# Optimization experiments

Hardware: AMD Instinct MI355X
Metric: run time of the kernel (lower is better)

Reference implementation:

```python
import jax, jax.numpy as jnp
import numpy as np

P_DROP = 0.3
TEMP = 1.0
UNC_THRESH = 0.3
TOP_K = 2
EXTRA_K = 2  # min(2, num_experts - top_k)
NUM_SAMPLES = 5


def setup_inputs() -> dict:
    key = jax.random.key(0)
    ks = jax.random.split(key, 7)
    B, D, H, E = 16384, 4096, 128, 64
    return {
        "x": jax.random.normal(ks[0], (B, D), jnp.float32),
        "W1": jax.random.normal(ks[1], (D, H), jnp.float32) / np.sqrt(D),
        "b1": jnp.zeros((H,), jnp.float32),
        "W2": jax.random.normal(ks[2], (H, E), jnp.float32) / np.sqrt(H),
        "b2": jnp.zeros((E,), jnp.float32),
        "mask1_u": jax.random.uniform(ks[3], (NUM_SAMPLES, B, H), jnp.float32),
        "mask2_u": jax.random.uniform(ks[4], (NUM_SAMPLES, B, E), jnp.float32),
    }


def reference(x, W1, b1, W2, b2, mask1_u, mask2_u):
    scale = 1.0 / (1.0 - P_DROP)
    # layer1: Linear -> ReLU -> Dropout; W1 is shared, so compute once and
    # apply per-sample dropout masks (identical math to the torch loop).
    h = jax.nn.relu(x @ W1 + b1)                              # [B, H]
    h = h[None] * ((mask1_u >= P_DROP).astype(h.dtype) * scale)  # [S, B, H]
    # layer2: Linear -> Dropout
    logits = jnp.einsum("sbh,he->sbe", h, W2) + b2            # [S, B, E]
    logits = logits * ((mask2_u >= P_DROP).astype(logits.dtype) * scale)

    mean_logits = logits.mean(axis=0)                          # [B, E]
    probs = jax.nn.softmax(mean_logits / TEMP, axis=-1)        # [B, E]
    all_probs = jax.nn.softmax(logits / TEMP, axis=-1)         # [S, B, E]
    # torch .std() is unbiased (ddof=1)
    uncertainty = jnp.std(all_probs, axis=0, ddof=1).mean(axis=-1)  # [B]

    # top_k + conditional expansion by EXTRA_K when uncertain.
    full_probs, full_idx = jax.lax.top_k(probs, TOP_K + EXTRA_K)
    topk_probs, topk_idx = full_probs[:, :TOP_K], full_idx[:, :TOP_K]
    uncertain = (uncertainty > UNC_THRESH)[:, None]
    extra_probs = jnp.where(uncertain, full_probs[:, TOP_K:], 0.0)
    extra_idx = jnp.where(uncertain, full_idx[:, TOP_K:], -1)
    out_idx = jnp.concatenate([topk_idx, extra_idx], axis=1)       # [B, TOP_K+EXTRA_K]
    out_probs = jnp.concatenate([topk_probs, extra_probs], axis=1)
    return out_idx, out_probs, uncertainty
```

## Files before the change

kernel.cpp:

```cpp
#include <hip/hip_runtime.h>

typedef short short8 __attribute__((ext_vector_type(8)));
typedef float f32x4 __attribute__((ext_vector_type(4)));

#define B_ROWS 16384
#define SCALE 1.4285714285714286f

__device__ __forceinline__ float bf2f(unsigned short u) {
    return __uint_as_float(((unsigned)u) << 16);
}
__device__ __forceinline__ unsigned short f2bf(float f) {
    unsigned u = __float_as_uint(f);
    u += 0x7fffu + ((u >> 16) & 1u);
    return (unsigned short)(u >> 16);
}

__device__ __forceinline__ void gl_lds16(const void* g, void* l) {
    __builtin_amdgcn_global_load_lds(
        (const __attribute__((address_space(1))) unsigned int*)g,
        (__attribute__((address_space(3))) unsigned int*)l, 16, 0, 0);
}

__device__ __forceinline__ float wave_max(float v) {
    #pragma unroll
    for (int m = 1; m < 64; m <<= 1) v = fmaxf(v, __shfl_xor(v, m, 64));
    return v;
}
__device__ __forceinline__ float wave_sum(float v) {
    #pragma unroll
    for (int m = 1; m < 64; m <<= 1) v += __shfl_xor(v, m, 64);
    return v;
}

__global__ void k_prep(const float* __restrict__ w1,
                       unsigned short* __restrict__ w1h,
                       unsigned short* __restrict__ w1l) {
    int tid = blockIdx.x * 256 + threadIdx.x;
    int n = tid >> 12, k = tid & 4095;
    float v = w1[k * 128 + n];
    unsigned short hi = f2bf(v);
    w1h[tid] = hi;
    w1l[tid] = f2bf(v - bf2f(hi));
}

__global__ __launch_bounds__(256) void k_gemm(const float* __restrict__ x,
                                              const unsigned short* __restrict__ w1h,
                                              const unsigned short* __restrict__ w1l,
                                              const float* __restrict__ b1,
                                              float* __restrict__ hout) {
    __shared__ unsigned short sAh[2][32 * 64], sAl[2][32 * 64];
    __shared__ unsigned short sBh[2][128 * 64], sBl[2][128 * 64];
    const int t = threadIdx.x;
    const int w = t >> 6, lane = t & 63;
    const int l15 = lane & 15, l4 = lane >> 4;
    const int rowBase = blockIdx.x << 5;

    f32x4 acc[2][2];
    #pragma unroll
    for (int i = 0; i < 2; ++i)
        #pragma unroll
        for (int j = 0; j < 2; ++j) {
            f32x4 z = {0.f, 0.f, 0.f, 0.f};
            acc[i][j] = z;
        }

    const int am = t >> 3, as = t & 7;
    const int apc = as ^ (am & 7);

    auto stage = [&](int buf, int k0) {
        #pragma unroll
        for (int j = 0; j < 4; ++j) {
            int c = j * 256 + t;
            int n = c >> 3;
            int cl = (c & 7) ^ (n & 7);
            const size_t go = (size_t)n * 4096 + k0 + (cl << 3);
            gl_lds16(w1h + go, &sBh[buf][c << 3]);
            gl_lds16(w1l + go, &sBl[buf][c << 3]);
        }
        const float* src = x + ((size_t)(rowBase + am) << 12) + k0 + (as << 3);
        float4 a0 = *(const float4*)src;
        float4 a1 = *(const float4*)(src + 4);
        float av[8] = {a0.x, a0.y, a0.z, a0.w, a1.x, a1.y, a1.z, a1.w};
        short8 H, L;
        #pragma unroll
        for (int i = 0; i < 8; ++i) {
            unsigned short hi = f2bf(av[i]);
            H[i] = (short)hi;
            L[i] = (short)f2bf(av[i] - bf2f(hi));
        }
        *(short8*)&sAh[buf][((am << 3) + apc) << 3] = H;
        *(short8*)&sAl[buf][((am << 3) + apc) << 3] = L;
    };

    stage(0, 0);
    __syncthreads();
    for (int it = 0; it < 64; ++it) {
        int buf = it & 1;
        if (it + 1 < 64) stage(buf ^ 1, (it + 1) << 6);
        #pragma unroll
        for (int ks = 0; ks < 2; ++ks) {
            short8 ah[2], al[2], bh[2], bl[2];
            #pragma unroll
            for (int mf = 0; mf < 2; ++mf) {
                int rm = (mf << 4) + l15;
                int pc = ((ks << 2) + l4) ^ (rm & 7);
                ah[mf] = *(const short8*)&sAh[buf][(((rm << 3) + pc)) << 3];
                al[mf] = *(const short8*)&sAl[buf][(((rm << 3) + pc)) << 3];
            }
            #pragma unroll
            for (int nf = 0; nf < 2; ++nf) {
                int rn = (w << 5) + (nf << 4) + l15;
                int pc = ((ks << 2) + l4) ^ (rn & 7);
                bh[nf] = *(const short8*)&sBh[buf][(((rn << 3) + pc)) << 3];
                bl[nf] = *(const short8*)&sBl[buf][(((rn << 3) + pc)) << 3];
            }
            #pragma unroll
            for (int mf = 0; mf < 2; ++mf)
                #pragma unroll
                for (int nf = 0; nf < 2; ++nf) {
                    acc[mf][nf] = __builtin_amdgcn_mfma_f32_16x16x32_bf16(
                        ah[mf], bh[nf], acc[mf][nf], 0, 0, 0);
                    acc[mf][nf] = __builtin_amdgcn_mfma_f32_16x16x32_bf16(
                        ah[mf], bl[nf], acc[mf][nf], 0, 0, 0);
                    acc[mf][nf] = __builtin_amdgcn_mfma_f32_16x16x32_bf16(
                        al[mf], bh[nf], acc[mf][nf], 0, 0, 0);
                }
        }
        __syncthreads();
    }

    #pragma unroll
    for (int nf = 0; nf < 2; ++nf) {
        int col = (w << 5) + (nf << 4) + l15;
        float bias = b1[col];
        #pragma unroll
        for (int mf = 0; mf < 2; ++mf) {
            int r0 = rowBase + (mf << 4) + (l4 << 2);
            #pragma unroll
            for (int rr = 0; rr < 4; ++rr) {
                float v = acc[mf][nf][rr] + bias;
                hout[(size_t)(r0 + rr) * 128 + col] = v > 0.f ? v : 0.f;
            }
        }
    }
}

__global__ __launch_bounds__(640) void k_logits(const float* __restrict__ h,
                                                const float* __restrict__ w2,
                                                const float* __restrict__ b2,
                                                const float* __restrict__ m1,
                                                const float* __restrict__ m2,
                                                float* __restrict__ lg) {
    const int t = threadIdx.x;
    const int wave = t >> 6, lane = t & 63;
    const int eh = (wave >= 5) ? 1 : 0;
    const int s = wave - (eh ? 5 : 0);
    const int row = (blockIdx.x << 6) + lane;
    const int ebu = __builtin_amdgcn_readfirstlane(eh << 5);

    float acc[32];
    #pragma unroll
    for (int e = 0; e < 32; ++e) acc[e] = 0.f;

    const float* hp = h + (size_t)row * 128;
    const float* m1p = m1 + ((size_t)s * B_ROWS + row) * 128;
    const float* wp = w2 + ebu;

    for (int k = 0; k < 128; k += 4) {
        float4 h4 = *(const float4*)(hp + k);
        float4 mu = *(const float4*)(m1p + k);
        float hd0 = (mu.x >= 0.3f) ? h4.x * SCALE : 0.f;
        float hd1 = (mu.y >= 0.3f) ? h4.y * SCALE : 0.f;
        float hd2 = (mu.z >= 0.3f) ? h4.z * SCALE : 0.f;
        float hd3 = (mu.w >= 0.3f) ? h4.w * SCALE : 0.f;
        const float* wk = wp + (k << 6);
        #pragma unroll
        for (int e = 0; e < 32; ++e) acc[e] += hd0 * wk[e];
        #pragma unroll
        for (int e = 0; e < 32; ++e) acc[e] += hd1 * wk[64 + e];
        #pragma unroll
        for (int e = 0; e < 32; ++e) acc[e] += hd2 * wk[128 + e];
        #pragma unroll
        for (int e = 0; e < 32; ++e) acc[e] += hd3 * wk[192 + e];
    }

    const float* m2p = m2 + ((size_t)s * B_ROWS + row) * 64 + ebu;
    float* op = lg + ((size_t)s * B_ROWS + row) * 64 + ebu;
    #pragma unroll
    for (int e = 0; e < 32; ++e) {
        float lv = acc[e] + b2[ebu + e];
        acc[e] = (m2p[e] >= 0.3f) ? lv * SCALE : 0.f;
    }
    #pragma unroll
    for (int e = 0; e < 32; e += 4) {
        float4 v = make_float4(acc[e], acc[e + 1], acc[e + 2], acc[e + 3]);
        *(float4*)(op + e) = v;
    }
}

__global__ __launch_bounds__(256) void k_stats(const float* __restrict__ lg,
                                               float* __restrict__ out) {
    const int lane = threadIdx.x & 63;
    const int wv = threadIdx.x >> 6;
    const int row = (blockIdx.x << 2) + wv;

    float l[5], p[5];
    #pragma unroll
    for (int s = 0; s < 5; ++s)
        l[s] = lg[((size_t)s * B_ROWS + row) * 64 + lane];

    float ml = (((l[0] + l[1]) + l[2]) + l[3] + l[4]);
    ml = ((((l[0] + l[1]) + l[2]) + l[3]) + l[4]) / 5.0f;

    #pragma unroll
    for (int s = 0; s < 5; ++s) {
        float mx = wave_max(l[s]);
        float ev = expf(l[s] - mx);
        float sm = wave_sum(ev);
        p[s] = ev / sm;
    }

    float mx = wave_max(ml);
    float ev = expf(ml - mx);
    float sm = wave_sum(ev);
    float prob = ev / sm;

    float mean = ((((p[0] + p[1]) + p[2]) + p[3]) + p[4]) / 5.0f;
    float var = 0.f;
    #pragma unroll
    for (int s = 0; s < 5; ++s) { float d = p[s] - mean; var += d * d; }
    float sd = sqrtf(var * 0.25f);
    float unc = wave_sum(sd) / 64.0f;

    float pv = prob;
    float vv[4]; int vi[4];
    #pragma unroll
    for (int t4 = 0; t4 < 4; ++t4) {
        float bv = pv; int bi = lane;
        #pragma unroll
        for (int m = 1; m < 64; m <<= 1) {
            float ov = __shfl_xor(bv, m, 64);
            int oi = __shfl_xor(bi, m, 64);
            if (ov > bv || (ov == bv && oi < bi)) { bv = ov; bi = oi; }
        }
        vv[t4] = bv; vi[t4] = bi;
        if (lane == bi) pv = -1.f;
    }

    if (lane == 0) {
        bool ug = unc > 0.3f;
        float4 fi = make_float4((float)vi[0], (float)vi[1],
                                ug ? (float)vi[2] : -1.f,
                                ug ? (float)vi[3] : -1.f);
        *(float4*)(out + (size_t)row * 4) = fi;
        float4 fp = make_float4(vv[0], vv[1],
                                ug ? vv[2] : 0.f,
                                ug ? vv[3] : 0.f);
        *(float4*)(out + 65536 + (size_t)row * 4) = fp;
        out[131072 + row] = unc;
    }
}

extern "C" void kernel_launch(void* const* d_in, const int* in_sizes, int n_in,
                              void* d_out, int out_size, void* d_ws, size_t ws_size,
                              hipStream_t stream) {
    const float* x  = (const float*)d_in[0];
    const float* W1 = (const float*)d_in[1];
    const float* b1 = (const float*)d_in[2];
    const float* W2 = (const float*)d_in[3];
    const float* b2 = (const float*)d_in[4];
    const float* m1 = (const float*)d_in[5];
    const float* m2 = (const float*)d_in[6];
    float* out = (float*)d_out;
    char* ws = (char*)d_ws;

    unsigned short* w1h = (unsigned short*)ws;
    unsigned short* w1l = (unsigned short*)(ws + (1 << 20));
    float* h  = (float*)(ws + (2 << 20));
    float* lg = (float*)(ws + (10 << 20));

    k_prep  <<<2048, 256, 0, stream>>>(W1, w1h, w1l);
    k_gemm  <<<512,  256, 0, stream>>>(x, w1h, w1l, b1, h);
    k_logits<<<256,  640, 0, stream>>>(h, W2, b2, m1, m2, lg);
    k_stats <<<4096, 256, 0, stream>>>(lg, out);
}
```

Measured before the change: 497.6 us.

## Fuse logits and stats kernels, stage per-sample logits in LDS

Merges the layer-2 logits kernel and the softmax/uncertainty/top-k kernel into one kernel that keeps each block's 32 rows × 5 samples of logits in shared memory. This removes the global write and re-read of the [5,B,64] logits buffer and one kernel launch. The thread mapping also changes: each thread now handles one row and 8 experts across all 5 samples, so each h value is reused across samples. In exchange, grid size drops to 512 blocks of 256 threads, the block uses 40KB of LDS, and the stats phase runs rows sequentially per wave, which may reduce parallelism.

```diff
diff --git a/kernel.cpp b/kernel.cpp
--- a/kernel.cpp
+++ b/kernel.cpp
@@ -145,119 +145,135 @@
     }
 }
 
-__global__ __launch_bounds__(640) void k_logits(const float* __restrict__ h,
-                                                const float* __restrict__ w2,
-                                                const float* __restrict__ b2,
-                                                const float* __restrict__ m1,
-                                                const float* __restrict__ m2,
-                                                float* __restrict__ lg) {
+__global__ __launch_bounds__(256) void k_logstats(const float* __restrict__ h,
+                                                  const float* __restrict__ w2,
+                                                  const float* __restrict__ b2,
+                                                  const float* __restrict__ m1,
+                                                  const float* __restrict__ m2,
+                                                  float* __restrict__ out) {
+    __shared__ float lgs[5 * 32 * 64];
     const int t = threadIdx.x;
-    const int wave = t >> 6, lane = t & 63;
-    const int eh = (wave >= 5) ? 1 : 0;
-    const int s = wave - (eh ? 5 : 0);
-    const int row = (blockIdx.x << 6) + lane;
-    const int ebu = __builtin_amdgcn_readfirstlane(eh << 5);
-
-    float acc[32];
-    #pragma unroll
-    for (int e = 0; e < 32; ++e) acc[e] = 0.f;
+    const int lr = t >> 3;
+    const int eg = t & 7;
+    const int e0 = eg << 3;
+    const int rowBase = blockIdx.x << 5;
+    const int row = rowBase + lr;
+
+    float acc[5][8];
+    #pragma unroll
+    for (int s = 0; s < 5; ++s)
+        #pragma unroll
+        for (int e = 0; e < 8; ++e) acc[s][e] = 0.f;
 
     const float* hp = h + (size_t)row * 128;
-    const float* m1p = m1 + ((size_t)s * B_ROWS + row) * 128;
-    const float* wp = w2 + ebu;
+    const size_t m1row = (size_t)row * 128;
 
     for (int k = 0; k < 128; k += 4) {
         float4 h4 = *(const float4*)(hp + k);
-        float4 mu = *(const float4*)(m1p + k);
-        float hd0 = (mu.x >= 0.3f) ? h4.x * SCALE : 0.f;
-        float hd1 = (mu.y >= 0.3f) ? h4.y * SCALE : 0.f;
-        float hd2 = (mu.z >= 0.3f) ? h4.z * SCALE : 0.f;
-        float hd3 = (mu.w >= 0.3f) ? h4.w * SCALE : 0.f;
-        const float* wk = wp + (k << 6);
-        #pragma unroll
-        for (int e = 0; e < 32; ++e) acc[e] += hd0 * wk[e];
-        #pragma unroll
-        for (int e = 0; e < 32; ++e) acc[e] += hd1 * wk[64 + e];
-        #pragma unroll
-        for (int e = 0; e < 32; ++e) acc[e] += hd2 * wk[128 + e];
-        #pragma unroll
-        for (int e = 0; e < 32; ++e) acc[e] += hd3 * wk[192 + e];
-    }
-
-    const float* m2p = m2 + ((size_t)s * B_ROWS + row) * 64 + ebu;
-    float* op = lg + ((size_t)s * B_ROWS + row) * 64 + ebu;
-    #pragma unroll
-    for (int e = 0; e < 32; ++e) {
-        float lv = acc[e] + b2[ebu + e];
-        acc[e] = (m2p[e] >= 0.3f) ? lv * SCALE : 0.f;
-    }
-    #pragma unroll
-    for (int e = 0; e < 32; e += 4) {
-        float4 v = make_float4(acc[e], acc[e + 1], acc[e + 2], acc[e + 3]);
-        *(float4*)(op + e) = v;
-    }
-}
-
-__global__ __launch_bounds__(256) void k_stats(const float* __restrict__ lg,
-                                               float* __restrict__ out) {
-    const int lane = threadIdx.x & 63;
-    const int wv = threadIdx.x >> 6;
-    const int row = (blockIdx.x << 2) + wv;
-
-    float l[5], p[5];
-    #pragma unroll
-    for (int s = 0; s < 5; ++s)
-        l[s] = lg[((size_t)s * B_ROWS + row) * 64 + lane];
-
-    float ml = (((l[0] + l[1]) + l[2]) + l[3] + l[4]);
-    ml = ((((l[0] + l[1]) + l[2]) + l[3]) + l[4]) / 5.0f;
-
+        float hv[4] = {h4.x, h4.y, h4.z, h4.w};
+        float w2v[4][8];
+        #pragma unroll
+        for (int kk = 0; kk < 4; ++kk) {
+            float4 wa = *(const float4*)(w2 + (k + kk) * 64 + e0);
+            float4 wb = *(const float4*)(w2 + (k + kk) * 64 + e0 + 4);
+            w2v[kk][0] = wa.x; w2v[kk][1] = wa.y; w2v[kk][2] = wa.z; w2v[kk][3] = wa.w;
+            w2v[kk][4] = wb.x; w2v[kk][5] = wb.y; w2v[kk][6] = wb.z; w2v[kk][7] = wb.w;
+        }
+        #pragma unroll
+        for (int s = 0; s < 5; ++s) {
+            float4 mu = *(const float4*)(m1 + (size_t)s * B_ROWS * 128 + m1row + k);
+            float hd[4];
+            hd[0] = (mu.x >= 0.3f) ? hv[0] * SCALE : 0.f;
+            hd[1] = (mu.y >= 0.3f) ? hv[1] * SCALE : 0.f;
+            hd[2] = (mu.z >= 0.3f) ? hv[2] * SCALE : 0.f;
+            hd[3] = (mu.w >= 0.3f) ? hv[3] * SCALE : 0.f;
+            #pragma unroll
+            for (int kk = 0; kk < 4; ++kk)
+                #pragma unroll
+                for (int e = 0; e < 8; ++e)
+                    acc[s][e] += hd[kk] * w2v[kk][e];
+        }
+    }
+
+    float4 ba = *(const float4*)(b2 + e0);
+    float4 bb = *(const float4*)(b2 + e0 + 4);
+    float bv[8] = {ba.x, ba.y, ba.z, ba.w, bb.x, bb.y, bb.z, bb.w};
     #pragma unroll
     for (int s = 0; s < 5; ++s) {
-        float mx = wave_max(l[s]);
-        float ev = expf(l[s] - mx);
+        const float* m2p = m2 + ((size_t)s * B_ROWS + row) * 64 + e0;
+        float4 ma = *(const float4*)m2p;
+        float4 mb = *(const float4*)(m2p + 4);
+        float mk[8] = {ma.x, ma.y, ma.z, ma.w, mb.x, mb.y, mb.z, mb.w};
+        float lv[8];
+        #pragma unroll
+        for (int e = 0; e < 8; ++e) {
+            float v = acc[s][e] + bv[e];
+            lv[e] = (mk[e] >= 0.3f) ? v * SCALE : 0.f;
+        }
+        float* dst = &lgs[((s << 5) + lr) * 64 + e0];
+        *(float4*)dst = make_float4(lv[0], lv[1], lv[2], lv[3]);
+        *(float4*)(dst + 4) = make_float4(lv[4], lv[5], lv[6], lv[7]);
+    }
+    __syncthreads();
+
+    const int wv = t >> 6, lane = t & 63;
+    for (int r8 = 0; r8 < 8; ++r8) {
+        int r = (wv << 3) + r8;
+        float l[5], p[5];
+        #pragma unroll
+        for (int s = 0; s < 5; ++s)
+            l[s] = lgs[((s << 5) + r) * 64 + lane];
+
+        float ml = ((((l[0] + l[1]) + l[2]) + l[3]) + l[4]) / 5.0f;
+
+        #pragma unroll
+        for (int s = 0; s < 5; ++s) {
+            float mx = wave_max(l[s]);
+            float ev = expf(l[s] - mx);
+            float sm = wave_sum(ev);
+            p[s] = ev / sm;
+        }
+
+        float mx = wave_max(ml);
+        float ev = expf(ml - mx);
         float sm = wave_sum(ev);
-        p[s] = ev / sm;
-    }
-
-    float mx = wave_max(ml);
-    float ev = expf(ml - mx);
-    float sm = wave_sum(ev);
-    float prob = ev / sm;
-
-    float mean = ((((p[0] + p[1]) + p[2]) + p[3]) + p[4]) / 5.0f;
-    float var = 0.f;
-    #pragma unroll
-    for (int s = 0; s < 5; ++s) { float d = p[s] - mean; var += d * d; }
-    float sd = sqrtf(var * 0.25f);
-    float unc = wave_sum(sd) / 64.0f;
-
-    float pv = prob;
-    float vv[4]; int vi[4];
-    #pragma unroll
-    for (int t4 = 0; t4 < 4; ++t4) {
-        float bv = pv; int bi = lane;
-        #pragma unroll
-        for (int m = 1; m < 64; m <<= 1) {
-            float ov = __shfl_xor(bv, m, 64);
-            int oi = __shfl_xor(bi, m, 64);
-            if (ov > bv || (ov == bv && oi < bi)) { bv = ov; bi = oi; }
-        }
-        vv[t4] = bv; vi[t4] = bi;
-        if (lane == bi) pv = -1.f;
-    }
-
-    if (lane == 0) {
-        bool ug = unc > 0.3f;
-        float4 fi = make_float4((float)vi[0], (float)vi[1],
-                                ug ? (float)vi[2] : -1.f,
-                                ug ? (float)vi[3] : -1.f);
-        *(float4*)(out + (size_t)row * 4) = fi;
-        float4 fp = make_float4(vv[0], vv[1],
-                                ug ? vv[2] : 0.f,
-                                ug ? vv[3] : 0.f);
-        *(float4*)(out + 65536 + (size_t)row * 4) = fp;
-        out[131072 + row] = unc;
+        float prob = ev / sm;
+
+        float mean = ((((p[0] + p[1]) + p[2]) + p[3]) + p[4]) / 5.0f;
+        float var = 0.f;
+        #pragma unroll
+        for (int s = 0; s < 5; ++s) { float d = p[s] - mean; var += d * d; }
+        float sd = sqrtf(var * 0.25f);
+        float unc = wave_sum(sd) / 64.0f;
+
+        float pv = prob;
+        float vv[4]; int vi[4];
+        #pragma unroll
+        for (int t4 = 0; t4 < 4; ++t4) {
+            float bvx = pv; int bi = lane;
+            #pragma unroll
+            for (int m = 1; m < 64; m <<= 1) {
+                float ov = __shfl_xor(bvx, m, 64);
+                int oi = __shfl_xor(bi, m, 64);
+                if (ov > bvx || (ov == bvx && oi < bi)) { bvx = ov; bi = oi; }
+            }
+            vv[t4] = bvx; vi[t4] = bi;
+            if (lane == bi) pv = -1.f;
+        }
+
+        if (lane == 0) {
+            int grow = rowBase + r;
+            bool ug = unc > 0.3f;
+            float4 fi = make_float4((float)vi[0], (float)vi[1],
+                                    ug ? (float)vi[2] : -1.f,
+                                    ug ? (float)vi[3] : -1.f);
+            *(float4*)(out + (size_t)grow * 4) = fi;
+            float4 fp = make_float4(vv[0], vv[1],
+                                    ug ? vv[2] : 0.f,
+                                    ug ? vv[3] : 0.f);
+            *(float4*)(out + 65536 + (size_t)grow * 4) = fp;
+            out[131072 + grow] = unc;
+        }
     }
 }
 
@@ -276,11 +292,9 @@
 
     unsigned short* w1h = (unsigned short*)ws;
     unsigned short* w1l = (unsigned short*)(ws + (1 << 20));
-    float* h  = (float*)(ws + (2 << 20));
-    float* lg = (float*)(ws + (10 << 20));
-
-    k_prep  <<<2048, 256, 0, stream>>>(W1, w1h, w1l);
-    k_gemm  <<<512,  256, 0, stream>>>(x, w1h, w1l, b1, h);
-    k_logits<<<256,  640, 0, stream>>>(h, W2, b2, m1, m2, lg);
-    k_stats <<<4096, 256, 0, stream>>>(lg, out);
-}
+    float* h = (float*)(ws + (2 << 20));
+
+    k_prep    <<<2048, 256, 0, stream>>>(W1, w1h, w1l);
+    k_gemm    <<<512,  256, 0, stream>>>(x, w1h, w1l, b1, h);
+    k_logstats<<<512,  256, 0, stream>>>(h, W2, b2, m1, m2, out);
+}
```

Measured after the change: 497.5 us. Within noise of the previous version (-0.0%).
